# Kernel optimization log

Measured on AMD Instinct MI355X. Metric: run time of the kernel, lower is better.

## Reference

```python
import jax, jax.numpy as jnp
import numpy as np

N, H, C, K, D = 16384, 16, 192, 43, 2
SIGMA = 1.0   # radius == sigma in Block
BN_EPS = 1e-5


def setup_inputs() -> dict:
    key = jax.random.key(0)
    ks = jax.random.split(key, 8)
    coord = jax.random.uniform(ks[0], (N, 3), dtype=jnp.float32)
    feat = jax.random.normal(ks[1], (N, C), dtype=jnp.float32)
    ref_idx = jax.random.randint(ks[2], (N, H), 0, N)
    # kernel point dispositions, within radius
    kp = jax.random.normal(ks[3], (K, 3), dtype=jnp.float32) * (0.3 * SIGMA)
    W1 = jax.random.normal(ks[4], (D, C, C), dtype=jnp.float32) / np.sqrt(C)
    Wk = jax.random.normal(ks[5], (D, K, C), dtype=jnp.float32) / np.sqrt(K * H)
    W3 = jax.random.normal(ks[6], (D, C, C), dtype=jnp.float32) / np.sqrt(C)
    ones = jnp.ones((D, C), jnp.float32)
    zeros = jnp.zeros((D, C), jnp.float32)
    return {
        "coord": coord, "feat": feat, "ref_idx": ref_idx, "kp": kp,
        "W1": W1, "Wk": Wk, "W3": W3,
        "g1": ones, "b1": zeros, "g2": ones, "b2": zeros, "g3": ones, "b3": zeros,
    }


def _bn(x, g, b):
    # PointBatchNorm on [N, C]: batch statistics over the point axis
    m = jnp.mean(x, axis=0)
    v = jnp.var(x, axis=0)
    return (x - m) * jax.lax.rsqrt(v + BN_EPS) * g + b


def reference(coord, feat, ref_idx, kp, W1, Wk, W3, g1, b1, g2, b2, g3, b3):
    # --- KP influence, shared across blocks (same coords / neighbor table) ---
    nb = coord[ref_idx] - coord[:, None, :]                       # [N,H,3] relative neighbor coords
    d2 = (jnp.sum(nb * nb, -1)[..., None]
          + jnp.sum(kp * kp, -1)[None, None, :]
          - 2.0 * jnp.einsum('nhd,kd->nhk', nb, kp))              # [N,H,K]
    d = jnp.sqrt(jnp.maximum(d2, 0.0))
    infl = jnp.maximum(1.0 - d / SIGMA, 0.0)                      # linear influence [N,H,K]

    relu = jax.nn.relu
    depth = W1.shape[0]
    for i in range(depth):
        identity = feat
        h = relu(_bn(feat @ W1[i], g1[i], b1[i]))                 # fc1 + BN + ReLU
        # KPConvD: depthwise kernel-point conv
        A = jnp.einsum('nhk,kc->nhc', infl, Wk[i])                # influence-projected depthwise weights
        h = jnp.einsum('nhc,nhc->nc', h[ref_idx], A)              # gather + weighted aggregate
        h = relu(_bn(h, g2[i], b2[i]))
        h = _bn(h @ W3[i], g3[i], b3[i])                          # fc3 + BN
        feat = relu(identity + h)                                 # skip + ReLU
    return feat
```

## Files before the change

### kernel.cpp

```cpp
#include <hip/hip_runtime.h>

#define N_PTS 16384
#define NH 16
#define NC 192
#define NK 43
#define ND 2
#define BN_EPS 1e-5f

typedef __attribute__((ext_vector_type(8))) short bf16x8;
typedef __attribute__((ext_vector_type(4))) float f32x4;

static __device__ __forceinline__ short f2bf(float f) {
    union { float f; unsigned u; } x; x.f = f;
    unsigned r = x.u + (0x7fffu + ((x.u >> 16) & 1u));
    return (short)(r >> 16);
}
static __device__ __forceinline__ float bf2f(short s) {
    union { unsigned u; float f; } x; x.u = ((unsigned)(unsigned short)s) << 16;
    return x.f;
}

__global__ __launch_bounds__(64) void k_wfrag(const float* __restrict__ W1,
                                              const float* __restrict__ Wk,
                                              const float* __restrict__ W3,
                                              short* __restrict__ Wb) {
    int b = blockIdx.x;
    int d = b / 168, r = b % 168;
    const float* src; short* dst; int kb, Ks, tile;
    if (r < 72)      { src = W1 + d * NC * NC; dst = Wb + d * 86016;         kb = 6; Ks = NC; tile = r; }
    else if (r < 96) { src = Wk + d * NK * NC; dst = Wb + d * 86016 + 36864; kb = 2; Ks = NK; tile = r - 72; }
    else             { src = W3 + d * NC * NC; dst = Wb + d * 86016 + 49152; kb = 6; Ks = NC; tile = r - 96; }
    int nt = tile / kb, ks = tile % kb;
    int lane = threadIdx.x, quad = lane >> 4, cl = lane & 15;
    bf16x8 vv;
#pragma unroll
    for (int j = 0; j < 8; ++j) {
        int k = ks * 32 + quad * 8 + j;
        vv[j] = (k < Ks) ? f2bf(src[k * NC + nt * 16 + cl]) : (short)0;
    }
    *(bf16x8*)(dst + ((nt * kb + ks) * 64 + lane) * 8) = vv;
}

__global__ __launch_bounds__(128) void k_stat2(const float* __restrict__ part, int nb,
                                               const float* __restrict__ g,
                                               const float* __restrict__ b,
                                               float* __restrict__ a_out,
                                               float* __restrict__ s_out) {
    __shared__ float red2[2];
    const int c = blockIdx.x;
    const int tid = threadIdx.x;
    const int lane = tid & 63;
    const int half = tid >> 6;
    const float* src = part + (half ? 192 + c : c);
    float s = 0.f;
    for (int i = lane; i < nb; i += 64) s += src[i * 384];
    s += __shfl_xor(s, 1);  s += __shfl_xor(s, 2);  s += __shfl_xor(s, 4);
    s += __shfl_xor(s, 8);  s += __shfl_xor(s, 16); s += __shfl_xor(s, 32);
    if (lane == 0) red2[half] = s;
    __syncthreads();
    if (tid == 0) {
        float m = red2[0] * (1.f / N_PTS);
        float var = red2[1] * (1.f / N_PTS) - m * m;
        float rs = rsqrtf(var + BN_EPS);
        float a = rs * g[c];
        a_out[c] = a;
        s_out[c] = b[c] - m * a;
    }
}

__global__ __launch_bounds__(192) void k_stat1b(const short* __restrict__ A,
                                                float* __restrict__ part) {
    __shared__ float red[8][384];
    const int tid = threadIdx.x;
    const int g = tid / 24, m = tid % 24;
    float s8[8], q8[8];
#pragma unroll
    for (int j = 0; j < 8; ++j) { s8[j] = 0.f; q8[j] = 0.f; }
#pragma unroll
    for (int p = 0; p < 4; ++p) {
        int row = blockIdx.x * 32 + p * 8 + g;
        bf16x8 v = *(const bf16x8*)(A + row * NC + m * 8);
#pragma unroll
        for (int j = 0; j < 8; ++j) {
            float x = bf2f(v[j]);
            s8[j] += x; q8[j] = fmaf(x, x, q8[j]);
        }
    }
#pragma unroll
    for (int j = 0; j < 8; ++j) {
        red[g][m * 8 + j] = s8[j];
        red[g][192 + m * 8 + j] = q8[j];
    }
    __syncthreads();
    float S = 0.f, Q = 0.f;
#pragma unroll
    for (int gg = 0; gg < 8; ++gg) { S += red[gg][tid]; Q += red[gg][192 + tid]; }
    part[blockIdx.x * 384 + tid] = S;
    part[blockIdx.x * 384 + 192 + tid] = Q;
}

__global__ __launch_bounds__(256) void k_gemm1(const float* __restrict__ feat,
                                               const short* __restrict__ T2prev,
                                               const float* __restrict__ st3prev,
                                               short* __restrict__ X1,
                                               const short* __restrict__ W1b,
                                               short* __restrict__ T,
                                               float* __restrict__ part) {
    __shared__ float red[4][384];
    const int tid = threadIdx.x;
    const int wave = tid >> 6, lane = tid & 63;
    const int quad = lane >> 4, cl = lane & 15;
    const int r0 = blockIdx.x * 64 + wave * 16;
    const int row = r0 + cl;

    f32x4 acc[12];
#pragma unroll
    for (int nt = 0; nt < 12; ++nt) acc[nt] = (f32x4){0.f, 0.f, 0.f, 0.f};

#pragma unroll
    for (int ks = 0; ks < 6; ++ks) {
        const int k0 = ks * 32 + quad * 8;
        const float* ap = feat + row * NC + k0;
        float4 a0 = *(const float4*)ap;
        float4 a1v = *(const float4*)(ap + 4);
        float x[8] = {a0.x, a0.y, a0.z, a0.w, a1v.x, a1v.y, a1v.z, a1v.w};
        if (T2prev) {
            bf16x8 t2 = *(const bf16x8*)(T2prev + row * NC + k0);
            float4 pa0 = *(const float4*)(st3prev + k0), pa1 = *(const float4*)(st3prev + k0 + 4);
            float4 ps0 = *(const float4*)(st3prev + 192 + k0), ps1 = *(const float4*)(st3prev + 192 + k0 + 4);
            float pav[8] = {pa0.x, pa0.y, pa0.z, pa0.w, pa1.x, pa1.y, pa1.z, pa1.w};
            float psv[8] = {ps0.x, ps0.y, ps0.z, ps0.w, ps1.x, ps1.y, ps1.z, ps1.w};
#pragma unroll
            for (int j = 0; j < 8; ++j)
                x[j] = fmaxf(x[j] + fmaf(pav[j], bf2f(t2[j]), psv[j]), 0.f);
        }
        bf16x8 af;
#pragma unroll
        for (int j = 0; j < 8; ++j) af[j] = f2bf(x[j]);
        if (T2prev) *(bf16x8*)(X1 + row * NC + k0) = af;
#pragma unroll
        for (int nt = 0; nt < 12; ++nt) {
            bf16x8 bf = *(const bf16x8*)(W1b + ((nt * 6 + ks) * 64 + lane) * 8);
            acc[nt] = __builtin_amdgcn_mfma_f32_16x16x32_bf16(af, bf, acc[nt], 0, 0, 0);
        }
    }
#pragma unroll
    for (int nt = 0; nt < 12; ++nt) {
        int c = nt * 16 + cl;
        float s = 0.f, sq = 0.f;
#pragma unroll
        for (int r = 0; r < 4; ++r) {
            float v = acc[nt][r];
            T[(r0 + quad * 4 + r) * NC + c] = f2bf(v);
            s += v; sq = fmaf(v, v, sq);
        }
        s += __shfl_xor(s, 16); s += __shfl_xor(s, 32);
        sq += __shfl_xor(sq, 16); sq += __shfl_xor(sq, 32);
        if (quad == 0) { red[wave][c] = s; red[wave][192 + c] = sq; }
    }
    __syncthreads();
    for (int t = tid; t < 384; t += 256)
        part[blockIdx.x * 384 + t] = red[0][t] + red[1][t] + red[2][t] + red[3][t];
}

__global__ __launch_bounds__(512) void k_kpconv(const float* __restrict__ coord,
                                                const int* __restrict__ ridx,
                                                const float* __restrict__ kp,
                                                const short* __restrict__ Wkb,
                                                const short* __restrict__ T,
                                                const float* __restrict__ st1,
                                                short* __restrict__ U) {
    __shared__ __align__(16) short wk_s[12288];
    __shared__ __align__(16) float4 kp_s[64];
    __shared__ float a1s[192], s1s[192];

    const int tid = threadIdx.x;
    {
        const float4* src = (const float4*)Wkb;
        float4* dst = (float4*)wk_s;
        for (int j = tid; j < 1536; j += 512) dst[j] = src[j];
        if (tid < 64) {
            bool ok = tid < NK;
            float x = ok ? kp[tid * 3 + 0] : 1e9f;
            float y = ok ? kp[tid * 3 + 1] : 1e9f;
            float z = ok ? kp[tid * 3 + 2] : 1e9f;
            kp_s[tid] = (float4){x, y, z, fmaf(x, x, fmaf(y, y, z * z))};
        }
        if (tid < 192) { a1s[tid] = st1[tid]; s1s[tid] = st1[192 + tid]; }
    }
    __syncthreads();

    const int wave = tid >> 6, lane = tid & 63;
    const int quad = lane >> 4, cl = lane & 15;
    const int n = blockIdx.x * 8 + wave;

    int idh = 0; float nbx = 0.f, nby = 0.f, nbz = 0.f;
    if (lane < NH) {
        idh = ridx[n * NH + lane];
        float cx = coord[n * 3 + 0], cy = coord[n * 3 + 1], cz = coord[n * 3 + 2];
        nbx = coord[idh * 3 + 0] - cx;
        nby = coord[idh * 3 + 1] - cy;
        nbz = coord[idh * 3 + 2] - cz;
    }
    const float nx = __shfl(nbx, cl), ny = __shfl(nby, cl), nz = __shfl(nbz, cl);
    int rowb[4];
#pragma unroll
    for (int r = 0; r < 4; ++r) rowb[r] = __shfl(idh, quad * 4 + r) * NC;

    unsigned short xv[12][4];
    const unsigned short* Tu = (const unsigned short*)T;
#pragma unroll
    for (int nt = 0; nt < 12; ++nt)
#pragma unroll
        for (int r = 0; r < 4; ++r)
            xv[nt][r] = Tu[rowb[r] + nt * 16 + cl];

    const float nb2 = fmaf(nx, nx, fmaf(ny, ny, nz * nz));
    const float m2x = -2.f * nx, m2y = -2.f * ny, m2z = -2.f * nz;
    bf16x8 af[2];
#pragma unroll
    for (int ks = 0; ks < 2; ++ks) {
#pragma unroll
        for (int j = 0; j < 8; ++j) {
            int k = ks * 32 + quad * 8 + j;
            float4 kpv = kp_s[k];
            float t = nb2 + kpv.w;
            t = fmaf(m2x, kpv.x, t);
            t = fmaf(m2y, kpv.y, t);
            t = fmaf(m2z, kpv.z, t);
            float d = sqrtf(fmaxf(t, 0.f));
            af[ks][j] = f2bf(fmaxf(1.f - d, 0.f));
        }
    }

    f32x4 acc[12];
#pragma unroll
    for (int nt = 0; nt < 12; ++nt) {
        bf16x8 b0 = *(const bf16x8*)(wk_s + ((nt * 2 + 0) * 64 + lane) * 8);
        bf16x8 b1v = *(const bf16x8*)(wk_s + ((nt * 2 + 1) * 64 + lane) * 8);
        f32x4 z = (f32x4){0.f, 0.f, 0.f, 0.f};
        z = __builtin_amdgcn_mfma_f32_16x16x32_bf16(af[0], b0, z, 0, 0, 0);
        acc[nt] = __builtin_amdgcn_mfma_f32_16x16x32_bf16(af[1], b1v, z, 0, 0, 0);
    }

#pragma unroll
    for (int nt = 0; nt < 12; ++nt) {
        const float a1c = a1s[nt * 16 + cl], s1c = s1s[nt * 16 + cl];
        float u = 0.f;
#pragma unroll
        for (int r = 0; r < 4; ++r) {
            float t = bf2f((short)xv[nt][r]);
            float x = fmaxf(fmaf(a1c, t, s1c), 0.f);
            u = fmaf(acc[nt][r], x, u);
        }
        u += __shfl_xor(u, 16);
        u += __shfl_xor(u, 32);
        if (quad == 0) U[n * NC + nt * 16 + cl] = f2bf(u);
    }
}

__global__ __launch_bounds__(256) void k_gemm3(const short* __restrict__ U,
                                               const float* __restrict__ st2,
                                               const short* __restrict__ W3b,
                                               short* __restrict__ T2,
                                               float* __restrict__ part) {
    __shared__ float red[4][384];
    const int tid = threadIdx.x;
    const int wave = tid >> 6, lane = tid & 63;
    const int quad = lane >> 4, cl = lane & 15;
    const int r0 = blockIdx.x * 64 + wave * 16;
    const int row = r0 + cl;

    f32x4 acc[12];
#pragma unroll
    for (int nt = 0; nt < 12; ++nt) acc[nt] = (f32x4){0.f, 0.f, 0.f, 0.f};

#pragma unroll
    for (int ks = 0; ks < 6; ++ks) {
        const int k0 = ks * 32 + quad * 8;
        bf16x8 u8 = *(const bf16x8*)(U + row * NC + k0);
        float4 aa0 = *(const float4*)(st2 + k0), aa1 = *(const float4*)(st2 + k0 + 4);
        float4 ss0 = *(const float4*)(st2 + 192 + k0), ss1 = *(const float4*)(st2 + 192 + k0 + 4);
        float av[8] = {aa0.x, aa0.y, aa0.z, aa0.w, aa1.x, aa1.y, aa1.z, aa1.w};
        float sv[8] = {ss0.x, ss0.y, ss0.z, ss0.w, ss1.x, ss1.y, ss1.z, ss1.w};
        bf16x8 af;
#pragma unroll
        for (int j = 0; j < 8; ++j)
            af[j] = f2bf(fmaxf(fmaf(av[j], bf2f(u8[j]), sv[j]), 0.f));
#pragma unroll
        for (int nt = 0; nt < 12; ++nt) {
            bf16x8 bf = *(const bf16x8*)(W3b + ((nt * 6 + ks) * 64 + lane) * 8);
            acc[nt] = __builtin_amdgcn_mfma_f32_16x16x32_bf16(af, bf, acc[nt], 0, 0, 0);
        }
    }
#pragma unroll
    for (int nt = 0; nt < 12; ++nt) {
        int c = nt * 16 + cl;
        float s = 0.f, sq = 0.f;
#pragma unroll
        for (int r = 0; r < 4; ++r) {
            float v = acc[nt][r];
            T2[(r0 + quad * 4 + r) * NC + c] = f2bf(v);
            s += v; sq = fmaf(v, v, sq);
        }
        s += __shfl_xor(s, 16); s += __shfl_xor(s, 32);
        sq += __shfl_xor(sq, 16); sq += __shfl_xor(sq, 32);
        if (quad == 0) { red[wave][c] = s; red[wave][192 + c] = sq; }
    }
    __syncthreads();
    for (int t = tid; t < 384; t += 256)
        part[blockIdx.x * 384 + t] = red[0][t] + red[1][t] + red[2][t] + red[3][t];
}

__global__ __launch_bounds__(256) void k_final(const short* __restrict__ T2,
                                               const float* __restrict__ st3,
                                               const short* __restrict__ X1,
                                               float* __restrict__ out) {
    const int i = blockIdx.x * 256 + threadIdx.x;
    const int c0 = (i * 8) % 192;
    bf16x8 t2 = *(const bf16x8*)(T2 + (long)i * 8);
    bf16x8 x1 = *(const bf16x8*)(X1 + (long)i * 8);
    float4 aa0 = *(const float4*)(st3 + c0), aa1 = *(const float4*)(st3 + c0 + 4);
    float4 ss0 = *(const float4*)(st3 + 192 + c0), ss1 = *(const float4*)(st3 + 192 + c0 + 4);
    float av[8] = {aa0.x, aa0.y, aa0.z, aa0.w, aa1.x, aa1.y, aa1.z, aa1.w};
    float sv[8] = {ss0.x, ss0.y, ss0.z, ss0.w, ss1.x, ss1.y, ss1.z, ss1.w};
    float4 o0, o1;
    float o[8];
#pragma unroll
    for (int j = 0; j < 8; ++j)
        o[j] = fmaxf(bf2f(x1[j]) + fmaf(av[j], bf2f(t2[j]), sv[j]), 0.f);
    o0 = (float4){o[0], o[1], o[2], o[3]};
    o1 = (float4){o[4], o[5], o[6], o[7]};
    *(float4*)(out + (long)i * 8)     = o0;
    *(float4*)(out + (long)i * 8 + 4) = o1;
}

extern "C" void kernel_launch(void* const* d_in, const int* in_sizes, int n_in,
                              void* d_out, int out_size, void* d_ws, size_t ws_size,
                              hipStream_t stream) {
    const float* coord = (const float*)d_in[0];
    const float* feat  = (const float*)d_in[1];
    const int*   ridx  = (const int*)d_in[2];
    const float* kp    = (const float*)d_in[3];
    const float* W1    = (const float*)d_in[4];
    const float* Wk    = (const float*)d_in[5];
    const float* W3    = (const float*)d_in[6];
    const float* g1    = (const float*)d_in[7];
    const float* b1    = (const float*)d_in[8];
    const float* g2    = (const float*)d_in[9];
    const float* b2    = (const float*)d_in[10];
    const float* g3    = (const float*)d_in[11];
    const float* b3    = (const float*)d_in[12];
    float* out = (float*)d_out;

    float* part  = (float*)d_ws;
    float* stats = part + 512 * 384;
    short* X1 = (short*)(stats + 2304);
    short* T  = X1 + N_PTS * NC;
    short* U  = T + N_PTS * NC;
    short* T2 = U + N_PTS * NC;
    short* Wb = T2 + N_PTS * NC;

    k_wfrag<<<336, 64, 0, stream>>>(W1, Wk, W3, Wb);

    for (int d = 0; d < ND; ++d) {
        const short* W1b = Wb + d * 86016;
        const short* Wkb = W1b + 36864;
        const short* W3b = W1b + 49152;
        float* st1 = stats + (d * 3 + 0) * 384;
        float* st2 = stats + (d * 3 + 1) * 384;
        float* st3 = stats + (d * 3 + 2) * 384;

        k_gemm1<<<256, 256, 0, stream>>>(feat,
                                         d ? T2 : (short*)nullptr,
                                         stats + 2 * 384,
                                         X1, W1b, T, part);
        k_stat2<<<192, 128, 0, stream>>>(part, 256, g1 + d * NC, b1 + d * NC, st1, st1 + 192);
        k_kpconv<<<N_PTS / 8, 512, 0, stream>>>(coord, ridx, kp, Wkb, T, st1, U);
        k_stat1b<<<512, 192, 0, stream>>>(U, part);
        k_stat2<<<192, 128, 0, stream>>>(part, 512, g2 + d * NC, b2 + d * NC, st2, st2 + 192);
        k_gemm3<<<256, 256, 0, stream>>>(U, st2, W3b, T2, part);
        k_stat2<<<192, 128, 0, stream>>>(part, 256, g3 + d * NC, b3 + d * NC, st3, st3 + 192);
    }
    k_final<<<N_PTS * NC / 8 / 256, 256, 0, stream>>>(T2, stats + 5 * 384, X1, out);
}
```

Before: 266.4 us.

## Fuse BN statistics into producer kernels via atomics and drop stat kernels

Removes the separate stat-reduction kernels: producers atomically accumulate per-channel sums and squares into a zeroed workspace, and consumers compute the BN scale and shift from them in their prologue. The kpconv kernel now handles 4 points per wave and accumulates U statistics itself, which eliminates the extra pass over U. This cuts the launches per block from 7 to 3 and removes partial-buffer traffic. In exchange it adds float atomics, which make the sums order-nondeterministic, and leaves fewer kpconv blocks in flight.

```diff
diff --git a/kernel.cpp b/kernel.cpp
--- a/kernel.cpp
+++ b/kernel.cpp
@@ -23,7 +23,11 @@
 __global__ __launch_bounds__(64) void k_wfrag(const float* __restrict__ W1,
                                               const float* __restrict__ Wk,
                                               const float* __restrict__ W3,
-                                              short* __restrict__ Wb) {
+                                              short* __restrict__ Wb,
+                                              float* __restrict__ stacc) {
+    int z = blockIdx.x * 64 + threadIdx.x;
+    if (z < 2304) stacc[z] = 0.f;
+
     int b = blockIdx.x;
     int d = b / 168, r = b % 168;
     const float* src; short* dst; int kb, Ks, tile;
@@ -41,77 +45,33 @@
     *(bf16x8*)(dst + ((nt * kb + ks) * 64 + lane) * 8) = vv;
 }
 
-__global__ __launch_bounds__(128) void k_stat2(const float* __restrict__ part, int nb,
-                                               const float* __restrict__ g,
-                                               const float* __restrict__ b,
-                                               float* __restrict__ a_out,
-                                               float* __restrict__ s_out) {
-    __shared__ float red2[2];
-    const int c = blockIdx.x;
-    const int tid = threadIdx.x;
-    const int lane = tid & 63;
-    const int half = tid >> 6;
-    const float* src = part + (half ? 192 + c : c);
-    float s = 0.f;
-    for (int i = lane; i < nb; i += 64) s += src[i * 384];
-    s += __shfl_xor(s, 1);  s += __shfl_xor(s, 2);  s += __shfl_xor(s, 4);
-    s += __shfl_xor(s, 8);  s += __shfl_xor(s, 16); s += __shfl_xor(s, 32);
-    if (lane == 0) red2[half] = s;
-    __syncthreads();
-    if (tid == 0) {
-        float m = red2[0] * (1.f / N_PTS);
-        float var = red2[1] * (1.f / N_PTS) - m * m;
-        float rs = rsqrtf(var + BN_EPS);
-        float a = rs * g[c];
-        a_out[c] = a;
-        s_out[c] = b[c] - m * a;
-    }
-}
-
-__global__ __launch_bounds__(192) void k_stat1b(const short* __restrict__ A,
-                                                float* __restrict__ part) {
-    __shared__ float red[8][384];
-    const int tid = threadIdx.x;
-    const int g = tid / 24, m = tid % 24;
-    float s8[8], q8[8];
-#pragma unroll
-    for (int j = 0; j < 8; ++j) { s8[j] = 0.f; q8[j] = 0.f; }
-#pragma unroll
-    for (int p = 0; p < 4; ++p) {
-        int row = blockIdx.x * 32 + p * 8 + g;
-        bf16x8 v = *(const bf16x8*)(A + row * NC + m * 8);
-#pragma unroll
-        for (int j = 0; j < 8; ++j) {
-            float x = bf2f(v[j]);
-            s8[j] += x; q8[j] = fmaf(x, x, q8[j]);
-        }
-    }
-#pragma unroll
-    for (int j = 0; j < 8; ++j) {
-        red[g][m * 8 + j] = s8[j];
-        red[g][192 + m * 8 + j] = q8[j];
-    }
-    __syncthreads();
-    float S = 0.f, Q = 0.f;
-#pragma unroll
-    for (int gg = 0; gg < 8; ++gg) { S += red[gg][tid]; Q += red[gg][192 + tid]; }
-    part[blockIdx.x * 384 + tid] = S;
-    part[blockIdx.x * 384 + 192 + tid] = Q;
-}
-
 __global__ __launch_bounds__(256) void k_gemm1(const float* __restrict__ feat,
                                                const short* __restrict__ T2prev,
-                                               const float* __restrict__ st3prev,
+                                               const float* __restrict__ st3acc,
+                                               const float* __restrict__ g3,
+                                               const float* __restrict__ b3,
                                                short* __restrict__ X1,
                                                const short* __restrict__ W1b,
                                                short* __restrict__ T,
-                                               float* __restrict__ part) {
+                                               float* __restrict__ st1acc) {
     __shared__ float red[4][384];
+    __shared__ float pa_s[192], ps_s[192];
     const int tid = threadIdx.x;
     const int wave = tid >> 6, lane = tid & 63;
     const int quad = lane >> 4, cl = lane & 15;
     const int r0 = blockIdx.x * 64 + wave * 16;
     const int row = r0 + cl;
+
+    if (T2prev) {
+        if (tid < 192) {
+            float m = st3acc[tid] * (1.f / N_PTS);
+            float v = st3acc[192 + tid] * (1.f / N_PTS) - m * m;
+            float a = rsqrtf(v + BN_EPS) * g3[tid];
+            pa_s[tid] = a;
+            ps_s[tid] = b3[tid] - m * a;
+        }
+        __syncthreads();
+    }
 
     f32x4 acc[12];
 #pragma unroll
@@ -126,13 +86,9 @@
         float x[8] = {a0.x, a0.y, a0.z, a0.w, a1v.x, a1v.y, a1v.z, a1v.w};
         if (T2prev) {
             bf16x8 t2 = *(const bf16x8*)(T2prev + row * NC + k0);
-            float4 pa0 = *(const float4*)(st3prev + k0), pa1 = *(const float4*)(st3prev + k0 + 4);
-            float4 ps0 = *(const float4*)(st3prev + 192 + k0), ps1 = *(const float4*)(st3prev + 192 + k0 + 4);
-            float pav[8] = {pa0.x, pa0.y, pa0.z, pa0.w, pa1.x, pa1.y, pa1.z, pa1.w};
-            float psv[8] = {ps0.x, ps0.y, ps0.z, ps0.w, ps1.x, ps1.y, ps1.z, ps1.w};
 #pragma unroll
             for (int j = 0; j < 8; ++j)
-                x[j] = fmaxf(x[j] + fmaf(pav[j], bf2f(t2[j]), psv[j]), 0.f);
+                x[j] = fmaxf(x[j] + fmaf(pa_s[k0 + j], bf2f(t2[j]), ps_s[k0 + j]), 0.f);
         }
         bf16x8 af;
 #pragma unroll
@@ -160,7 +116,7 @@
     }
     __syncthreads();
     for (int t = tid; t < 384; t += 256)
-        part[blockIdx.x * 384 + t] = red[0][t] + red[1][t] + red[2][t] + red[3][t];
+        atomicAdd(&st1acc[t], red[0][t] + red[1][t] + red[2][t] + red[3][t]);
 }
 
 __global__ __launch_bounds__(512) void k_kpconv(const float* __restrict__ coord,
@@ -168,11 +124,15 @@
                                                 const float* __restrict__ kp,
                                                 const short* __restrict__ Wkb,
                                                 const short* __restrict__ T,
-                                                const float* __restrict__ st1,
-                                                short* __restrict__ U) {
+                                                const float* __restrict__ st1acc,
+                                                const float* __restrict__ g1,
+                                                const float* __restrict__ b1,
+                                                short* __restrict__ U,
+                                                float* __restrict__ st2acc) {
     __shared__ __align__(16) short wk_s[12288];
     __shared__ __align__(16) float4 kp_s[64];
     __shared__ float a1s[192], s1s[192];
+    __shared__ float red[8][384];
 
     const int tid = threadIdx.x;
     {
@@ -186,91 +146,134 @@
             float z = ok ? kp[tid * 3 + 2] : 1e9f;
             kp_s[tid] = (float4){x, y, z, fmaf(x, x, fmaf(y, y, z * z))};
         }
-        if (tid < 192) { a1s[tid] = st1[tid]; s1s[tid] = st1[192 + tid]; }
+        if (tid < 192) {
+            float m = st1acc[tid] * (1.f / N_PTS);
+            float v = st1acc[192 + tid] * (1.f / N_PTS) - m * m;
+            float a = rsqrtf(v + BN_EPS) * g1[tid];
+            a1s[tid] = a;
+            s1s[tid] = b1[tid] - m * a;
+        }
     }
     __syncthreads();
 
     const int wave = tid >> 6, lane = tid & 63;
     const int quad = lane >> 4, cl = lane & 15;
-    const int n = blockIdx.x * 8 + wave;
-
-    int idh = 0; float nbx = 0.f, nby = 0.f, nbz = 0.f;
-    if (lane < NH) {
-        idh = ridx[n * NH + lane];
-        float cx = coord[n * 3 + 0], cy = coord[n * 3 + 1], cz = coord[n * 3 + 2];
-        nbx = coord[idh * 3 + 0] - cx;
-        nby = coord[idh * 3 + 1] - cy;
-        nbz = coord[idh * 3 + 2] - cz;
-    }
-    const float nx = __shfl(nbx, cl), ny = __shfl(nby, cl), nz = __shfl(nbz, cl);
-    int rowb[4];
-#pragma unroll
-    for (int r = 0; r < 4; ++r) rowb[r] = __shfl(idh, quad * 4 + r) * NC;
-
-    unsigned short xv[12][4];
-    const unsigned short* Tu = (const unsigned short*)T;
-#pragma unroll
-    for (int nt = 0; nt < 12; ++nt)
-#pragma unroll
-        for (int r = 0; r < 4; ++r)
-            xv[nt][r] = Tu[rowb[r] + nt * 16 + cl];
-
-    const float nb2 = fmaf(nx, nx, fmaf(ny, ny, nz * nz));
-    const float m2x = -2.f * nx, m2y = -2.f * ny, m2z = -2.f * nz;
-    bf16x8 af[2];
-#pragma unroll
-    for (int ks = 0; ks < 2; ++ks) {
-#pragma unroll
-        for (int j = 0; j < 8; ++j) {
-            int k = ks * 32 + quad * 8 + j;
-            float4 kpv = kp_s[k];
-            float t = nb2 + kpv.w;
-            t = fmaf(m2x, kpv.x, t);
-            t = fmaf(m2y, kpv.y, t);
-            t = fmaf(m2z, kpv.z, t);
-            float d = sqrtf(fmaxf(t, 0.f));
-            af[ks][j] = f2bf(fmaxf(1.f - d, 0.f));
-        }
-    }
-
-    f32x4 acc[12];
-#pragma unroll
-    for (int nt = 0; nt < 12; ++nt) {
-        bf16x8 b0 = *(const bf16x8*)(wk_s + ((nt * 2 + 0) * 64 + lane) * 8);
-        bf16x8 b1v = *(const bf16x8*)(wk_s + ((nt * 2 + 1) * 64 + lane) * 8);
-        f32x4 z = (f32x4){0.f, 0.f, 0.f, 0.f};
-        z = __builtin_amdgcn_mfma_f32_16x16x32_bf16(af[0], b0, z, 0, 0, 0);
-        acc[nt] = __builtin_amdgcn_mfma_f32_16x16x32_bf16(af[1], b1v, z, 0, 0, 0);
-    }
-
-#pragma unroll
-    for (int nt = 0; nt < 12; ++nt) {
-        const float a1c = a1s[nt * 16 + cl], s1c = s1s[nt * 16 + cl];
-        float u = 0.f;
-#pragma unroll
-        for (int r = 0; r < 4; ++r) {
-            float t = bf2f((short)xv[nt][r]);
-            float x = fmaxf(fmaf(a1c, t, s1c), 0.f);
-            u = fmaf(acc[nt][r], x, u);
-        }
-        u += __shfl_xor(u, 16);
-        u += __shfl_xor(u, 32);
-        if (quad == 0) U[n * NC + nt * 16 + cl] = f2bf(u);
+
+    float s2[12], q2[12];
+#pragma unroll
+    for (int nt = 0; nt < 12; ++nt) { s2[nt] = 0.f; q2[nt] = 0.f; }
+
+#pragma unroll 1
+    for (int p = 0; p < 4; ++p) {
+        const int n = blockIdx.x * 32 + wave * 4 + p;
+
+        int idh = 0; float nbx = 0.f, nby = 0.f, nbz = 0.f;
+        if (lane < NH) {
+            idh = ridx[n * NH + lane];
+            float cx = coord[n * 3 + 0], cy = coord[n * 3 + 1], cz = coord[n * 3 + 2];
+            nbx = coord[idh * 3 + 0] - cx;
+            nby = coord[idh * 3 + 1] - cy;
+            nbz = coord[idh * 3 + 2] - cz;
+        }
+        const float nx = __shfl(nbx, cl), ny = __shfl(nby, cl), nz = __shfl(nbz, cl);
+        int rowb[4];
+#pragma unroll
+        for (int r = 0; r < 4; ++r) rowb[r] = __shfl(idh, quad * 4 + r) * NC;
+
+        unsigned short xv[12][4];
+        const unsigned short* Tu = (const unsigned short*)T;
+#pragma unroll
+        for (int nt = 0; nt < 12; ++nt)
+#pragma unroll
+            for (int r = 0; r < 4; ++r)
+                xv[nt][r] = Tu[rowb[r] + nt * 16 + cl];
+
+        const float nb2 = fmaf(nx, nx, fmaf(ny, ny, nz * nz));
+        const float m2x = -2.f * nx, m2y = -2.f * ny, m2z = -2.f * nz;
+        bf16x8 af[2];
+#pragma unroll
+        for (int ks = 0; ks < 2; ++ks) {
+#pragma unroll
+            for (int j = 0; j < 8; ++j) {
+                int k = ks * 32 + quad * 8 + j;
+                float4 kpv = kp_s[k];
+                float t = nb2 + kpv.w;
+                t = fmaf(m2x, kpv.x, t);
+                t = fmaf(m2y, kpv.y, t);
+                t = fmaf(m2z, kpv.z, t);
+                float d = sqrtf(fmaxf(t, 0.f));
+                af[ks][j] = f2bf(fmaxf(1.f - d, 0.f));
+            }
+        }
+
+        f32x4 acc[12];
+#pragma unroll
+        for (int nt = 0; nt < 12; ++nt) {
+            bf16x8 b0 = *(const bf16x8*)(wk_s + ((nt * 2 + 0) * 64 + lane) * 8);
+            bf16x8 b1v = *(const bf16x8*)(wk_s + ((nt * 2 + 1) * 64 + lane) * 8);
+            f32x4 z = (f32x4){0.f, 0.f, 0.f, 0.f};
+            z = __builtin_amdgcn_mfma_f32_16x16x32_bf16(af[0], b0, z, 0, 0, 0);
+            acc[nt] = __builtin_amdgcn_mfma_f32_16x16x32_bf16(af[1], b1v, z, 0, 0, 0);
+        }
+
+#pragma unroll
+        for (int nt = 0; nt < 12; ++nt) {
+            const float a1c = a1s[nt * 16 + cl], s1c = s1s[nt * 16 + cl];
+            float u = 0.f;
+#pragma unroll
+            for (int r = 0; r < 4; ++r) {
+                float t = bf2f((short)xv[nt][r]);
+                float x = fmaxf(fmaf(a1c, t, s1c), 0.f);
+                u = fmaf(acc[nt][r], x, u);
+            }
+            u += __shfl_xor(u, 16);
+            u += __shfl_xor(u, 32);
+            s2[nt] += u;
+            q2[nt] = fmaf(u, u, q2[nt]);
+            if (quad == 0) U[n * NC + nt * 16 + cl] = f2bf(u);
+        }
+    }
+
+    if (quad == 0) {
+#pragma unroll
+        for (int nt = 0; nt < 12; ++nt) {
+            red[wave][nt * 16 + cl] = s2[nt];
+            red[wave][192 + nt * 16 + cl] = q2[nt];
+        }
+    }
+    __syncthreads();
+    if (tid < 384) {
+        float S = 0.f;
+#pragma unroll
+        for (int w = 0; w < 8; ++w) S += red[w][tid];
+        atomicAdd(&st2acc[tid], S);
     }
 }
 
 __global__ __launch_bounds__(256) void k_gemm3(const short* __restrict__ U,
-                                               const float* __restrict__ st2,
+                                               const float* __restrict__ st2acc,
+                                               const float* __restrict__ g2,
+                                               const float* __restrict__ b2,
                                                const short* __restrict__ W3b,
                                                short* __restrict__ T2,
-                                               float* __restrict__ part) {
+                                               float* __restrict__ st3acc) {
     __shared__ float red[4][384];
+    __shared__ float a2s[192], s2s[192];
     const int tid = threadIdx.x;
     const int wave = tid >> 6, lane = tid & 63;
     const int quad = lane >> 4, cl = lane & 15;
     const int r0 = blockIdx.x * 64 + wave * 16;
     const int row = r0 + cl;
 
+    if (tid < 192) {
+        float m = st2acc[tid] * (1.f / N_PTS);
+        float v = st2acc[192 + tid] * (1.f / N_PTS) - m * m;
+        float a = rsqrtf(v + BN_EPS) * g2[tid];
+        a2s[tid] = a;
+        s2s[tid] = b2[tid] - m * a;
+    }
+    __syncthreads();
+
     f32x4 acc[12];
 #pragma unroll
     for (int nt = 0; nt < 12; ++nt) acc[nt] = (f32x4){0.f, 0.f, 0.f, 0.f};
@@ -279,14 +282,10 @@
     for (int ks = 0; ks < 6; ++ks) {
         const int k0 = ks * 32 + quad * 8;
         bf16x8 u8 = *(const bf16x8*)(U + row * NC + k0);
-        float4 aa0 = *(const float4*)(st2 + k0), aa1 = *(const float4*)(st2 + k0 + 4);
-        float4 ss0 = *(const float4*)(st2 + 192 + k0), ss1 = *(const float4*)(st2 + 192 + k0 + 4);
-        float av[8] = {aa0.x, aa0.y, aa0.z, aa0.w, aa1.x, aa1.y, aa1.z, aa1.w};
-        float sv[8] = {ss0.x, ss0.y, ss0.z, ss0.w, ss1.x, ss1.y, ss1.z, ss1.w};
         bf16x8 af;
 #pragma unroll
         for (int j = 0; j < 8; ++j)
-            af[j] = f2bf(fmaxf(fmaf(av[j], bf2f(u8[j]), sv[j]), 0.f));
+            af[j] = f2bf(fmaxf(fmaf(a2s[k0 + j], bf2f(u8[j]), s2s[k0 + j]), 0.f));
 #pragma unroll
         for (int nt = 0; nt < 12; ++nt) {
             bf16x8 bf = *(const bf16x8*)(W3b + ((nt * 6 + ks) * 64 + lane) * 8);
@@ -309,30 +308,35 @@
     }
     __syncthreads();
     for (int t = tid; t < 384; t += 256)
-        part[blockIdx.x * 384 + t] = red[0][t] + red[1][t] + red[2][t] + red[3][t];
+        atomicAdd(&st3acc[t], red[0][t] + red[1][t] + red[2][t] + red[3][t]);
 }
 
 __global__ __launch_bounds__(256) void k_final(const short* __restrict__ T2,
-                                               const float* __restrict__ st3,
+                                               const float* __restrict__ st3acc,
+                                               const float* __restrict__ g3,
+                                               const float* __restrict__ b3,
                                                const short* __restrict__ X1,
                                                float* __restrict__ out) {
+    __shared__ float a3s[192], s3s[192];
+    if (threadIdx.x < 192) {
+        float m = st3acc[threadIdx.x] * (1.f / N_PTS);
+        float v = st3acc[192 + threadIdx.x] * (1.f / N_PTS) - m * m;
+        float a = rsqrtf(v + BN_EPS) * g3[threadIdx.x];
+        a3s[threadIdx.x] = a;
+        s3s[threadIdx.x] = b3[threadIdx.x] - m * a;
+    }
+    __syncthreads();
+
     const int i = blockIdx.x * 256 + threadIdx.x;
     const int c0 = (i * 8) % 192;
     bf16x8 t2 = *(const bf16x8*)(T2 + (long)i * 8);
     bf16x8 x1 = *(const bf16x8*)(X1 + (long)i * 8);
-    float4 aa0 = *(const float4*)(st3 + c0), aa1 = *(const float4*)(st3 + c0 + 4);
-    float4 ss0 = *(const float4*)(st3 + 192 + c0), ss1 = *(const float4*)(st3 + 192 + c0 + 4);
-    float av[8] = {aa0.x, aa0.y, aa0.z, aa0.w, aa1.x, aa1.y, aa1.z, aa1.w};
-    float sv[8] = {ss0.x, ss0.y, ss0.z, ss0.w, ss1.x, ss1.y, ss1.z, ss1.w};
-    float4 o0, o1;
     float o[8];
 #pragma unroll
     for (int j = 0; j < 8; ++j)
-        o[j] = fmaxf(bf2f(x1[j]) + fmaf(av[j], bf2f(t2[j]), sv[j]), 0.f);
-    o0 = (float4){o[0], o[1], o[2], o[3]};
-    o1 = (float4){o[4], o[5], o[6], o[7]};
-    *(float4*)(out + (long)i * 8)     = o0;
-    *(float4*)(out + (long)i * 8 + 4) = o1;
+        o[j] = fmaxf(bf2f(x1[j]) + fmaf(a3s[c0 + j], bf2f(t2[j]), s3s[c0 + j]), 0.f);
+    *(float4*)(out + (long)i * 8)     = (float4){o[0], o[1], o[2], o[3]};
+    *(float4*)(out + (long)i * 8 + 4) = (float4){o[4], o[5], o[6], o[7]};
 }
 
 extern "C" void kernel_launch(void* const* d_in, const int* in_sizes, int n_in,
@@ -353,34 +357,34 @@
     const float* b3    = (const float*)d_in[12];
     float* out = (float*)d_out;
 
-    float* part  = (float*)d_ws;
-    float* stats = part + 512 * 384;
-    short* X1 = (short*)(stats + 2304);
+    float* stacc = (float*)d_ws;
+    short* X1 = (short*)(stacc + 2304);
     short* T  = X1 + N_PTS * NC;
     short* U  = T + N_PTS * NC;
     short* T2 = U + N_PTS * NC;
     short* Wb = T2 + N_PTS * NC;
 
-    k_wfrag<<<336, 64, 0, stream>>>(W1, Wk, W3, Wb);
+    k_wfrag<<<336, 64, 0, stream>>>(W1, Wk, W3, Wb, stacc);
 
     for (int d = 0; d < ND; ++d) {
         const short* W1b = Wb + d * 86016;
         const short* Wkb = W1b + 36864;
         const short* W3b = W1b + 49152;
-        float* st1 = stats + (d * 3 + 0) * 384;
-        float* st2 = stats + (d * 3 + 1) * 384;
-        float* st3 = stats + (d * 3 + 2) * 384;
+        float* st1acc = stacc + (d * 3 + 0) * 384;
+        float* st2acc = stacc + (d * 3 + 1) * 384;
+        float* st3acc = stacc + (d * 3 + 2) * 384;
 
         k_gemm1<<<256, 256, 0, stream>>>(feat,
                                          d ? T2 : (short*)nullptr,
-                                         stats + 2 * 384,
-                                         X1, W1b, T, part);
-        k_stat2<<<192, 128, 0, stream>>>(part, 256, g1 + d * NC, b1 + d * NC, st1, st1 + 192);
-        k_kpconv<<<N_PTS / 8, 512, 0, stream>>>(coord, ridx, kp, Wkb, T, st1, U);
-        k_stat1b<<<512, 192, 0, stream>>>(U, part);
-        k_stat2<<<192, 128, 0, stream>>>(part, 512, g2 + d * NC, b2 + d * NC, st2, st2 + 192);
-        k_gemm3<<<256, 256, 0, stream>>>(U, st2, W3b, T2, part);
-        k_stat2<<<192, 128, 0, stream>>>(part, 256, g3 + d * NC, b3 + d * NC, st3, st3 + 192);
-    }
-    k_final<<<N_PTS * NC / 8 / 256, 256, 0, stream>>>(T2, stats + 5 * 384, X1, out);
-}
+                                         stacc + 2 * 384,
+                                         g3, b3,
+                                         X1, W1b, T, st1acc);
+        k_kpconv<<<512, 512, 0, stream>>>(coord, ridx, kp, Wkb, T,
+                                          st1acc, g1 + d * NC, b1 + d * NC,
+                                          U, st2acc);
+        k_gemm3<<<256, 256, 0, stream>>>(U, st2acc, g2 + d * NC, b2 + d * NC,
+                                         W3b, T2, st3acc);
+    }
+    k_final<<<N_PTS * NC / 8 / 256, 256, 0, stream>>>(T2, stacc + 5 * 384,
+                                                      g3 + NC, b3 + NC, X1, out);
+}
```

Result: slower. 341.4 us (+28.2%).
